# Performance work log

Hardware: AMD Instinct MI355X
Metric: run time of the kernel (lower is better)

## Reference

```python
import jax, jax.numpy as jnp
import numpy as np

N_PREV = 65536
BATCH = 2048
DIM = 128


def setup_inputs() -> dict:
    key = jax.random.key(0)
    k1, k2 = jax.random.split(key)
    n = N_PREV + BATCH
    target_lib = jax.random.normal(k1, (n, DIM), dtype=jnp.float32)
    reached_lib = jax.random.normal(k2, (n, DIM), dtype=jnp.float32)
    return {
        "target_goal_embedding_library": target_lib,
        "reached_goal_embedding_library": reached_lib,
        "batch_size": BATCH,
    }


def reference(target_goal_embedding_library, reached_goal_embedding_library, batch_size):
    # slice the library: last batch_size rows are current target/reached goals
    tg = target_goal_embedding_library[-batch_size:]      # [B, D]
    rg = reached_goal_embedding_library[-batch_size:]     # [B, D]
    prev = reached_goal_embedding_library[:-batch_size]   # [N_prev, D]

    # brute-force squared euclidean distances via gram trick: [B, N_prev]
    d2 = (
        jnp.sum(tg * tg, axis=-1, keepdims=True)
        - 2.0 * tg @ prev.T
        + jnp.sum(prev * prev, axis=-1)[None, :]
    )
    idx = jnp.argmin(d2, axis=1)          # top-1 nearest neighbor ids, [B]
    closest = prev[idx]                   # [B, D] gather

    # LP(g, s, r) = ||g - s|| - ||g - r||; value and grad wrt g, vmapped over batch
    def LP(g, s, r):
        return (
            jnp.sqrt(jnp.sum(jnp.square(g - s), axis=-1))
            - jnp.sqrt(jnp.sum(jnp.square(g - r), axis=-1))
        )

    IM_vals, IM_grads = jax.vmap(jax.value_and_grad(LP, 0), in_axes=(0, 0, 0))(
        tg, closest, rg
    )
    return IM_vals, IM_grads
```

## Files before the change

kernel.cpp:

```cpp
#include <hip/hip_runtime.h>
#include <math.h>

#define DIM 128
#define BATCH 2048
#define NPREV 65536
#define NCH 64
#define NJT 16
#define DELTA 0.8f

typedef __attribute__((ext_vector_type(8))) short bf16x8;
typedef __attribute__((ext_vector_type(4))) float f32x4;
typedef unsigned short u16;

static __device__ __forceinline__ unsigned short f2bf(float f) {
    unsigned int u = __float_as_uint(f);
    u += 0x7FFF + ((u >> 16) & 1);
    return (unsigned short)(u >> 16);
}

#define GLOAD16(g, l) __builtin_amdgcn_global_load_lds( \
    (const __attribute__((address_space(1))) void*)(g), \
    (__attribute__((address_space(3))) void*)(l), 16, 0, 0)

__global__ __launch_bounds__(256) void k_convB(const float* __restrict__ src,
                                               u16* __restrict__ dst,
                                               float* __restrict__ p2part) {
    int id = blockIdx.x * 256 + threadIdx.x;
    int img = id >> 9, c = id & 511;
    int ks2 = c >> 8, rem = c & 255, col = rem >> 2, slot = rem & 3;
    int koct = slot ^ ((col >> 1) & 3);
    int srow = (img >> 1) * 64 + col;
    int scol = (img & 1) * 64 + ks2 * 32 + koct * 8;
    const float* s = src + (size_t)srow * DIM + scol;
    float4 f0 = *reinterpret_cast<const float4*>(s);
    float4 f1 = *reinterpret_cast<const float4*>(s + 4);
    float f[8] = {f0.x, f0.y, f0.z, f0.w, f1.x, f1.y, f1.z, f1.w};
    union { unsigned short us[8]; uint4 v; } o;
    float sum = 0.f;
    #pragma unroll
    for (int e = 0; e < 8; ++e) { o.us[e] = f2bf(f[e]); sum += f[e] * f[e]; }
    *reinterpret_cast<uint4*>(dst + (size_t)id * 8) = o.v;
    p2part[srow * 16 + (scol >> 3)] = sum;
}

__global__ __launch_bounds__(256) void k_prev2r(const float* __restrict__ p2part,
                                                float* __restrict__ p2h) {
    int row = blockIdx.x * 256 + threadIdx.x;
    const float4* p = reinterpret_cast<const float4*>(p2part + (size_t)row * 16);
    float4 a = p[0], b = p[1], c = p[2], d = p[3];
    float s = ((a.x + a.y) + (a.z + a.w)) + ((b.x + b.y) + (b.z + b.w))
            + ((c.x + c.y) + (c.z + c.w)) + ((d.x + d.y) + (d.z + d.w));
    p2h[row] = -0.5f * s;
}

__global__ __launch_bounds__(256) void k_convA(const float* __restrict__ src,
                                               u16* __restrict__ dst) {
    int id = blockIdx.x * 256 + threadIdx.x;
    int img = id >> 10, c = id & 1023;
    int ks2 = c >> 9, rem = c & 511, row = rem >> 2, koct = rem & 3;
    int srow = (img >> 1) * 128 + row;
    int scol = (img & 1) * 64 + ks2 * 32 + koct * 8;
    const float* s = src + (size_t)srow * DIM + scol;
    float4 f0 = *reinterpret_cast<const float4*>(s);
    float4 f1 = *reinterpret_cast<const float4*>(s + 4);
    float f[8] = {f0.x, f0.y, f0.z, f0.w, f1.x, f1.y, f1.z, f1.w};
    union { unsigned short us[8]; uint4 v; } o;
    #pragma unroll
    for (int e = 0; e < 8; ++e) o.us[e] = f2bf(f[e]);
    *reinterpret_cast<uint4*>(dst + (size_t)id * 8) = o.v;
}

__global__ __launch_bounds__(256, 3) void k_gemm_argmin(
    const u16* __restrict__ Aimg, const u16* __restrict__ Bimg,
    const float* __restrict__ p2h, float4* __restrict__ partial)
{
    __shared__ __align__(16) u16 Bt[2][8192];

    const int t = threadIdx.x;
    const int lane = t & 63;
    const int w = t >> 6;
    const int wrow = w & 1;
    const int cg = w >> 1;
    const int l15 = lane & 15;
    const int lhi = lane >> 4;

    const int bid = blockIdx.x;
    const int mtile = bid >> 6;
    const int chunk = bid & 63;

    const u16* gb0 = Bimg + (size_t)chunk * NJT * 8192;

    #pragma unroll
    for (int c = 0; c < 4; ++c)
        GLOAD16(gb0 + c * 2048 + t * 8, &Bt[0][c * 2048 + t * 8]);

    bf16x8 areg[4][4];
    {
        const u16* ab = Aimg + (size_t)mtile * 2 * 8192;
        #pragma unroll
        for (int s = 0; s < 4; ++s) {
            const int img = s >> 1, ks2 = s & 1;
            #pragma unroll
            for (int fm = 0; fm < 4; ++fm) {
                int row = wrow * 64 + fm * 16 + l15;
                areg[s][fm] = *reinterpret_cast<const bf16x8*>(
                    ab + (size_t)img * 8192 + (ks2 * 512 + row * 4 + lhi) * 8);
            }
        }
    }

    const int bbase = (cg * 32 + l15) * 64 + ((lhi ^ ((l15 >> 1) & 3)) << 4);
    const unsigned sbase = ((unsigned)cg << 8) | (unsigned)l15;
    const int phbase = chunk * 1024 + cg * 32 + l15;
    const f32x4 z4 = {0.f, 0.f, 0.f, 0.f};

    float v1[4][4], v2[4][4];
    #pragma unroll
    for (int fm = 0; fm < 4; ++fm)
        #pragma unroll
        for (int r = 0; r < 4; ++r) { v1[fm][r] = -INFINITY; v2[fm][r] = -INFINITY; }

    float phc[2];
    phc[0] = p2h[phbase]; phc[1] = p2h[phbase + 16];

    for (int jt = 0; jt < NJT; ++jt) {
        const int p = jt & 1;
        __syncthreads();
        if (jt + 1 < NJT) {
            const u16* gb = gb0 + (size_t)(jt + 1) * 8192;
            u16* lb = Bt[p ^ 1];
            #pragma unroll
            for (int c = 0; c < 4; ++c)
                GLOAD16(gb + c * 2048 + t * 8, lb + c * 2048 + t * 8);
        }
        float phn[2];
        if (jt + 1 < NJT) {
            phn[0] = p2h[phbase + (jt + 1) * 64];
            phn[1] = p2h[phbase + (jt + 1) * 64 + 16];
        }

        f32x4 acc[4][2];
        const char* Bc = (const char*)Bt[p];
        __builtin_amdgcn_s_setprio(1);
        #pragma unroll
        for (int s = 0; s < 4; ++s) {
            const int h = s >> 1, ks2 = s & 1;
            bf16x8 bf[2];
            #pragma unroll
            for (int fn = 0; fn < 2; ++fn)
                bf[fn] = *reinterpret_cast<const bf16x8*>(
                    Bc + h * 8192 + ks2 * 4096 + fn * 1024 + bbase);
            if (s == 0) {
                #pragma unroll
                for (int fm = 0; fm < 4; ++fm)
                    #pragma unroll
                    for (int fn = 0; fn < 2; ++fn)
                        acc[fm][fn] = __builtin_amdgcn_mfma_f32_16x16x32_bf16(
                            areg[0][fm], bf[fn], z4, 0, 0, 0);
            } else {
                #pragma unroll
                for (int fm = 0; fm < 4; ++fm)
                    #pragma unroll
                    for (int fn = 0; fn < 2; ++fn)
                        acc[fm][fn] = __builtin_amdgcn_mfma_f32_16x16x32_bf16(
                            areg[s][fm], bf[fn], acc[fm][fn], 0, 0, 0);
            }
        }
        __builtin_amdgcn_s_setprio(0);

        const unsigned stampv = sbase | ((unsigned)jt << 4);
        #pragma unroll
        for (int fm = 0; fm < 4; ++fm) {
            #pragma unroll
            for (int r = 0; r < 4; ++r) {
                float s0 = acc[fm][0][r] + phc[0];
                float s1 = acc[fm][1][r] + phc[1];
                float m = fmaxf(s0, s1);
                float key = __uint_as_float((__float_as_uint(m) & ~0x7FFu) | stampv);
                float tm = fminf(v1[fm][r], key);
                v1[fm][r] = fmaxf(v1[fm][r], key);
                v2[fm][r] = fmaxf(v2[fm][r], tm);
            }
        }

        if (jt + 1 < NJT) { phc[0] = phn[0]; phc[1] = phn[1]; }
    }

    float2* red = reinterpret_cast<float2*>(Bt);
    #pragma unroll
    for (int fm = 0; fm < 4; ++fm) {
        #pragma unroll
        for (int r = 0; r < 4; ++r) {
            float a1 = v1[fm][r], a2 = v2[fm][r];
            #pragma unroll
            for (int m = 1; m < 16; m <<= 1) {
                float o1 = __shfl_xor(a1, m), o2 = __shfl_xor(a2, m);
                float n2 = fmaxf(fminf(a1, o1), fmaxf(a2, o2));
                a1 = fmaxf(a1, o1); a2 = n2;
            }
            if (l15 == 0) {
                int row = wrow * 64 + fm * 16 + lhi * 4 + r;
                red[row * 2 + cg] = make_float2(a1, a2);
            }
        }
    }
    __syncthreads();
    if (t < 128) {
        float2 x = red[t * 2 + 0], y = red[t * 2 + 1];
        float u1f = fmaxf(x.x, y.x);
        float u2f = fmaxf(fminf(x.x, y.x), fmaxf(x.y, y.y));
        unsigned ua = __float_as_uint(u1f), ub = __float_as_uint(u2f);
        int ja = chunk * 1024 + (int)((ua >> 4) & 15) * 64 + (int)((ua >> 8) & 1) * 32
               + (int)(ua & 15);
        int jb = chunk * 1024 + (int)((ub >> 4) & 15) * 64 + (int)((ub >> 8) & 1) * 32
               + (int)(ub & 15);
        float d1 = -2.0f * __uint_as_float(ua & ~0x7FFu);
        float d2 = -2.0f * __uint_as_float(ub & ~0x7FFu);
        partial[(size_t)(mtile * 128 + t) * NCH + chunk] =
            make_float4(d1, __int_as_float(ja), d2, __int_as_float(jb));
    }
}

__global__ __launch_bounds__(256) void k_final2(
    const float* __restrict__ tg, const float* __restrict__ rg,
    const float* __restrict__ prev, const float4* __restrict__ partial,
    float* __restrict__ out_vals, float* __restrict__ out_grads)
{
    const int wv = threadIdx.x >> 6, lane = threadIdx.x & 63;
    const int i = blockIdx.x * 4 + wv;
    const float4 e = partial[(size_t)i * NCH + lane];

    float bv = e.x;
    #pragma unroll
    for (int m = 1; m < 64; m <<= 1) bv = fminf(bv, __shfl_xor(bv, m));

    unsigned long long m1 = __ballot(e.x <= bv + DELTA);
    unsigned long long m2 = __ballot(e.z <= bv + DELTA);
    const float2 g = *reinterpret_cast<const float2*>(tg + (size_t)i * DIM + 2 * lane);
    const int j1i = __float_as_int(e.y), j2i = __float_as_int(e.w);

    float bestd = INFINITY; int bestj = 0x7fffffff;
    while (m1 | m2) {
        int j0;
        if (m1) { int src = __ffsll(m1) - 1; m1 &= m1 - 1; j0 = __shfl(j1i, src); }
        else    { int src = __ffsll(m2) - 1; m2 &= m2 - 1; j0 = __shfl(j2i, src); }
        #pragma unroll
        for (int f = 0; f < 2; ++f) {
            int cj = j0 + f * 16;
            const float2 p = *reinterpret_cast<const float2*>(prev + (size_t)cj * DIM + 2 * lane);
            float dx = g.x - p.x, dy = g.y - p.y;
            float d = dx * dx + dy * dy;
            #pragma unroll
            for (int m = 1; m < 64; m <<= 1) d += __shfl_xor(d, m);
            if (d < bestd || (d == bestd && cj < bestj)) { bestd = d; bestj = cj; }
        }
    }

    const float2 s = *reinterpret_cast<const float2*>(prev + (size_t)bestj * DIM + 2 * lane);
    const float2 r = *reinterpret_cast<const float2*>(rg + (size_t)i * DIM + 2 * lane);
    const float dsx = g.x - s.x, dsy = g.y - s.y;
    const float drx = g.x - r.x, dry = g.y - r.y;
    float ds = dsx * dsx + dsy * dsy;
    float dr = drx * drx + dry * dry;
    #pragma unroll
    for (int m = 1; m < 64; m <<= 1) { ds += __shfl_xor(ds, m); dr += __shfl_xor(dr, m); }
    const float sds = sqrtf(ds), sdr = sqrtf(dr);
    if (lane == 0) out_vals[i] = sds - sdr;
    const float is = 1.0f / sds, ir = 1.0f / sdr;
    float2 gr;
    gr.x = dsx * is - drx * ir;
    gr.y = dsy * is - dry * ir;
    *reinterpret_cast<float2*>(out_grads + (size_t)i * DIM + 2 * lane) = gr;
}

#define TM 128
#define TN 128
#define FNCHUNK 16
#define JT_PER_CHUNK 32

__global__ __launch_bounds__(256) void k_prev2(const float* __restrict__ prev,
                                               float* __restrict__ prev2,
                                               int nprev) {
    const int wave = threadIdx.x >> 6;
    const int lane = threadIdx.x & 63;
    const int row = blockIdx.x * 4 + wave;
    if (row >= nprev) return;
    const float2 v = *reinterpret_cast<const float2*>(prev + (size_t)row * DIM + 2 * lane);
    float s = v.x * v.x + v.y * v.y;
    #pragma unroll
    for (int m = 1; m < 64; m <<= 1) s += __shfl_xor(s, m);
    if (lane == 0) prev2[row] = s;
}

__global__ __launch_bounds__(256, 1) void k_argmin_fb(
    const float* __restrict__ tg, const float* __restrict__ prev,
    const float* __restrict__ prev2, float2* __restrict__ partial)
{
    __shared__ float4 tgL[TM * 32];
    __shared__ float4 pvL[TN * 32];
    __shared__ float  p2L[TN];
    const int t = threadIdx.x;
    const int rowTile = blockIdx.x;
    const int chunk = blockIdx.y;
    const float4* tgG = reinterpret_cast<const float4*>(tg + (size_t)rowTile * TM * DIM);
    #pragma unroll
    for (int i = 0; i < 16; ++i) {
        const int idx = t + 256 * i;
        const int row = idx >> 5, kk = idx & 31;
        tgL[row * 32 + (kk ^ (row & 7))] = tgG[idx];
    }
    const int tx = t & 15, ty = t >> 4;
    const int sa = ty & 7, sb = tx & 7;
    float minval[8]; int minidx[8];
    #pragma unroll
    for (int ri = 0; ri < 8; ++ri) { minval[ri] = INFINITY; minidx[ri] = 0x7fffffff; }
    const int jchunk0 = chunk * (JT_PER_CHUNK * TN);
    for (int jt = 0; jt < JT_PER_CHUNK; ++jt) {
        const int j0 = jchunk0 + jt * TN;
        __syncthreads();
        const float4* pvG = reinterpret_cast<const float4*>(prev + (size_t)j0 * DIM);
        #pragma unroll
        for (int i = 0; i < 16; ++i) {
            const int idx = t + 256 * i;
            const int row = idx >> 5, kk = idx & 31;
            pvL[row * 32 + (kk ^ (row & 7))] = pvG[idx];
        }
        if (t < TN) p2L[t] = prev2[j0 + t];
        __syncthreads();
        float acc[8][8];
        #pragma unroll
        for (int ri = 0; ri < 8; ++ri)
            #pragma unroll
            for (int ci = 0; ci < 8; ++ci) acc[ri][ci] = 0.f;
        #pragma unroll 2
        for (int kk = 0; kk < 32; ++kk) {
            float4 a[8], b[8];
            const int ka = kk ^ sa, kb = kk ^ sb;
            #pragma unroll
            for (int ri = 0; ri < 8; ++ri) a[ri] = tgL[(ty + 16 * ri) * 32 + ka];
            #pragma unroll
            for (int ci = 0; ci < 8; ++ci) b[ci] = pvL[(tx + 16 * ci) * 32 + kb];
            #pragma unroll
            for (int ri = 0; ri < 8; ++ri)
                #pragma unroll
                for (int ci = 0; ci < 8; ++ci) {
                    acc[ri][ci] += a[ri].x * b[ci].x;
                    acc[ri][ci] += a[ri].y * b[ci].y;
                    acc[ri][ci] += a[ri].z * b[ci].z;
                    acc[ri][ci] += a[ri].w * b[ci].w;
                }
        }
        #pragma unroll
        for (int ci = 0; ci < 8; ++ci) {
            const int jl = tx + 16 * ci;
            const int jg = j0 + jl;
            const float pj = p2L[jl];
            #pragma unroll
            for (int ri = 0; ri < 8; ++ri) {
                const float d = pj - 2.f * acc[ri][ci];
                if (d < minval[ri]) { minval[ri] = d; minidx[ri] = jg; }
            }
        }
    }
    __syncthreads();
    float2* red = reinterpret_cast<float2*>(pvL);
    #pragma unroll
    for (int ri = 0; ri < 8; ++ri) {
        const int row = ty + 16 * ri;
        red[row * 16 + tx] = make_float2(minval[ri], __int_as_float(minidx[ri]));
    }
    __syncthreads();
    if (t < TM) {
        float bv = INFINITY; int bi = 0x7fffffff;
        #pragma unroll
        for (int e = 0; e < 16; ++e) {
            const float2 p = red[t * 16 + e];
            const int pi = __float_as_int(p.y);
            if (p.x < bv || (p.x == bv && pi < bi)) { bv = p.x; bi = pi; }
        }
        partial[(size_t)(rowTile * TM + t) * FNCHUNK + chunk] =
            make_float2(bv, __int_as_float(bi));
    }
}

__global__ __launch_bounds__(256) void k_final_fb(
    const float* __restrict__ tg, const float* __restrict__ rg,
    const float* __restrict__ prev, const float2* __restrict__ partial,
    float* __restrict__ out_vals, float* __restrict__ out_grads)
{
    const int wave = threadIdx.x >> 6, lane = threadIdx.x & 63;
    const int i = blockIdx.x * 4 + wave;
    float bv = INFINITY; int bi = 0x7fffffff;
    if (lane < FNCHUNK) {
        const float2 p = partial[(size_t)i * FNCHUNK + lane];
        bv = p.x; bi = __float_as_int(p.y);
    }
    #pragma unroll
    for (int m = 1; m < 16; m <<= 1) {
        const float ov = __shfl_xor(bv, m);
        const int   oi = __shfl_xor(bi, m);
        if (ov < bv || (ov == bv && oi < bi)) { bv = ov; bi = oi; }
    }
    bi = __shfl(bi, 0);
    const float2 g = *reinterpret_cast<const float2*>(tg   + (size_t)i  * DIM + 2 * lane);
    const float2 s = *reinterpret_cast<const float2*>(prev + (size_t)bi * DIM + 2 * lane);
    const float2 r = *reinterpret_cast<const float2*>(rg   + (size_t)i  * DIM + 2 * lane);
    const float dsx = g.x - s.x, dsy = g.y - s.y;
    const float drx = g.x - r.x, dry = g.y - r.y;
    float ds = dsx * dsx + dsy * dsy;
    float dr = drx * drx + dry * dry;
    #pragma unroll
    for (int m = 1; m < 64; m <<= 1) { ds += __shfl_xor(ds, m); dr += __shfl_xor(dr, m); }
    const float sds = sqrtf(ds), sdr = sqrtf(dr);
    if (lane == 0) out_vals[i] = sds - sdr;
    const float is = 1.0f / sds, ir = 1.0f / sdr;
    float2 gr;
    gr.x = dsx * is - drx * ir;
    gr.y = dsy * is - dry * ir;
    *reinterpret_cast<float2*>(out_grads + (size_t)i * DIM + 2 * lane) = gr;
}

extern "C" void kernel_launch(void* const* d_in, const int* in_sizes, int n_in,
                              void* d_out, int out_size, void* d_ws, size_t ws_size,
                              hipStream_t stream) {
    const float* target  = (const float*)d_in[0];
    const float* reached = (const float*)d_in[1];
    const int n_total = in_sizes[0] / DIM;
    const int nprev = n_total - BATCH;

    const float* tg   = target  + (size_t)nprev * DIM;
    const float* rg   = reached + (size_t)nprev * DIM;
    const float* prev = reached;

    float* out_vals  = (float*)d_out;
    float* out_grads = out_vals + BATCH;

    const size_t offB  = 0;
    const size_t offA  = (size_t)2048 * 4096 * 2;
    const size_t offP2 = offA + (size_t)32 * 8192 * 2;
    const size_t offPP = offP2 + (size_t)NPREV * 4;
    const size_t offPt = offPP + (size_t)NPREV * 16 * 4;
    const size_t need  = offPt + (size_t)BATCH * NCH * sizeof(float4);

    if (nprev == NPREV && ws_size >= need) {
        u16*    Bb      = (u16*)((char*)d_ws + offB);
        u16*    Ab      = (u16*)((char*)d_ws + offA);
        float*  p2h     = (float*)((char*)d_ws + offP2);
        float*  p2part  = (float*)((char*)d_ws + offPP);
        float4* partial = (float4*)((char*)d_ws + offPt);

        k_convB<<<(2048 * 512) / 256, 256, 0, stream>>>(prev, Bb, p2part);
        k_convA<<<(32 * 1024) / 256, 256, 0, stream>>>(tg, Ab);
        k_prev2r<<<NPREV / 256, 256, 0, stream>>>(p2part, p2h);
        k_gemm_argmin<<<1024, 256, 0, stream>>>(Ab, Bb, p2h, partial);
        k_final2<<<BATCH / 4, 256, 0, stream>>>(tg, rg, prev, partial,
                                                out_vals, out_grads);
    } else {
        float*  prev2   = (float*)d_ws;
        float2* partial = (float2*)((char*)d_ws + (size_t)nprev * sizeof(float));
        k_prev2<<<nprev / 4, 256, 0, stream>>>(prev, prev2, nprev);
        dim3 grid(BATCH / TM, FNCHUNK);
        k_argmin_fb<<<grid, 256, 0, stream>>>(tg, prev, prev2, partial);
        k_final_fb<<<BATCH / 4, 256, 0, stream>>>(tg, rg, prev, partial, out_vals, out_grads);
    }
}
```

Measured before the change: 70.12 us.

## Load B fragments directly from global into registers, drop LDS staging

Rewrites the GEMM-argmin kernel so each wave owns a 64-row strip and streams pre-swizzled B fragments straight from global memory into registers with double-buffered banks, removing LDS, syncthreads and the cross-wave reduction. The B and A conversion kernels now emit data in exact MFMA fragment order. Each wave now covers 64 columns per tile (4 fn) and the argmin key tracks 16-column groups, so the final refinement checks 4 candidates per stamp instead of 2. Grid halves to 512 blocks with occupancy 2. This trades LDS sharing for more global/L2 traffic per wave and a costlier refinement.

```diff
diff --git a/kernel.cpp b/kernel.cpp
--- a/kernel.cpp
+++ b/kernel.cpp
@@ -5,7 +5,6 @@
 #define BATCH 2048
 #define NPREV 65536
 #define NCH 64
-#define NJT 16
 #define DELTA 0.8f
 
 typedef __attribute__((ext_vector_type(8))) short bf16x8;
@@ -18,22 +17,17 @@
     return (unsigned short)(u >> 16);
 }
 
-#define GLOAD16(g, l) __builtin_amdgcn_global_load_lds( \
-    (const __attribute__((address_space(1))) void*)(g), \
-    (__attribute__((address_space(3))) void*)(l), 16, 0, 0)
-
 __global__ __launch_bounds__(256) void k_convB(const float* __restrict__ src,
                                                u16* __restrict__ dst,
                                                float* __restrict__ p2part) {
     int id = blockIdx.x * 256 + threadIdx.x;
-    int img = id >> 9, c = id & 511;
-    int ks2 = c >> 8, rem = c & 255, col = rem >> 2, slot = rem & 3;
-    int koct = slot ^ ((col >> 1) & 3);
-    int srow = (img >> 1) * 64 + col;
-    int scol = (img & 1) * 64 + ks2 * 32 + koct * 8;
-    const float* s = src + (size_t)srow * DIM + scol;
-    float4 f0 = *reinterpret_cast<const float4*>(s);
-    float4 f1 = *reinterpret_cast<const float4*>(s + 4);
+    int lane = id & 63, frag = id >> 6;
+    int fn = frag & 3, s = (frag >> 2) & 3, jt = (frag >> 4) & 15, chunk = frag >> 8;
+    int srow = chunk * 1024 + jt * 64 + fn * 16 + (lane & 15);
+    int scol = (s >> 1) * 64 + (s & 1) * 32 + (lane >> 4) * 8;
+    const float* sp = src + (size_t)srow * DIM + scol;
+    float4 f0 = *reinterpret_cast<const float4*>(sp);
+    float4 f1 = *reinterpret_cast<const float4*>(sp + 4);
     float f[8] = {f0.x, f0.y, f0.z, f0.w, f1.x, f1.y, f1.z, f1.w};
     union { unsigned short us[8]; uint4 v; } o;
     float sum = 0.f;
@@ -56,13 +50,13 @@
 __global__ __launch_bounds__(256) void k_convA(const float* __restrict__ src,
                                                u16* __restrict__ dst) {
     int id = blockIdx.x * 256 + threadIdx.x;
-    int img = id >> 10, c = id & 1023;
-    int ks2 = c >> 9, rem = c & 511, row = rem >> 2, koct = rem & 3;
-    int srow = (img >> 1) * 128 + row;
-    int scol = (img & 1) * 64 + ks2 * 32 + koct * 8;
-    const float* s = src + (size_t)srow * DIM + scol;
-    float4 f0 = *reinterpret_cast<const float4*>(s);
-    float4 f1 = *reinterpret_cast<const float4*>(s + 4);
+    int lane = id & 63, frag = id >> 6;
+    int fm = frag & 3, s = (frag >> 2) & 3, strip = frag >> 4;
+    int srow = strip * 64 + fm * 16 + (lane & 15);
+    int scol = (s >> 1) * 64 + (s & 1) * 32 + (lane >> 4) * 8;
+    const float* sp = src + (size_t)srow * DIM + scol;
+    float4 f0 = *reinterpret_cast<const float4*>(sp);
+    float4 f1 = *reinterpret_cast<const float4*>(sp + 4);
     float f[8] = {f0.x, f0.y, f0.z, f0.w, f1.x, f1.y, f1.z, f1.w};
     union { unsigned short us[8]; uint4 v; } o;
     #pragma unroll
@@ -70,48 +64,32 @@
     *reinterpret_cast<uint4*>(dst + (size_t)id * 8) = o.v;
 }
 
-__global__ __launch_bounds__(256, 3) void k_gemm_argmin(
+__global__ __launch_bounds__(256, 2) void k_gemm_argmin(
     const u16* __restrict__ Aimg, const u16* __restrict__ Bimg,
     const float* __restrict__ p2h, float4* __restrict__ partial)
 {
-    __shared__ __align__(16) u16 Bt[2][8192];
-
     const int t = threadIdx.x;
     const int lane = t & 63;
     const int w = t >> 6;
-    const int wrow = w & 1;
-    const int cg = w >> 1;
     const int l15 = lane & 15;
     const int lhi = lane >> 4;
 
     const int bid = blockIdx.x;
-    const int mtile = bid >> 6;
     const int chunk = bid & 63;
-
-    const u16* gb0 = Bimg + (size_t)chunk * NJT * 8192;
-
-    #pragma unroll
-    for (int c = 0; c < 4; ++c)
-        GLOAD16(gb0 + c * 2048 + t * 8, &Bt[0][c * 2048 + t * 8]);
+    const int strip = (bid >> 6) * 4 + w;
 
     bf16x8 areg[4][4];
     {
-        const u16* ab = Aimg + (size_t)mtile * 2 * 8192;
-        #pragma unroll
-        for (int s = 0; s < 4; ++s) {
-            const int img = s >> 1, ks2 = s & 1;
-            #pragma unroll
-            for (int fm = 0; fm < 4; ++fm) {
-                int row = wrow * 64 + fm * 16 + l15;
-                areg[s][fm] = *reinterpret_cast<const bf16x8*>(
-                    ab + (size_t)img * 8192 + (ks2 * 512 + row * 4 + lhi) * 8);
-            }
-        }
-    }
-
-    const int bbase = (cg * 32 + l15) * 64 + ((lhi ^ ((l15 >> 1) & 3)) << 4);
-    const unsigned sbase = ((unsigned)cg << 8) | (unsigned)l15;
-    const int phbase = chunk * 1024 + cg * 32 + l15;
+        const u16* ab = Aimg + ((size_t)strip * 16) * 512 + (size_t)lane * 8;
+        #pragma unroll
+        for (int s = 0; s < 4; ++s)
+            #pragma unroll
+            for (int fm = 0; fm < 4; ++fm)
+                areg[s][fm] = *reinterpret_cast<const bf16x8*>(ab + (s * 4 + fm) * 512);
+    }
+
+    const u16* gb = Bimg + ((size_t)chunk * 256) * 512 + (size_t)lane * 8;
+    const int phbase = chunk * 1024 + l15;
     const f32x4 z4 = {0.f, 0.f, 0.f, 0.f};
 
     float v1[4][4], v2[4][4];
@@ -120,73 +98,78 @@
         #pragma unroll
         for (int r = 0; r < 4; ++r) { v1[fm][r] = -INFINITY; v2[fm][r] = -INFINITY; }
 
-    float phc[2];
-    phc[0] = p2h[phbase]; phc[1] = p2h[phbase + 16];
-
-    for (int jt = 0; jt < NJT; ++jt) {
-        const int p = jt & 1;
-        __syncthreads();
-        if (jt + 1 < NJT) {
-            const u16* gb = gb0 + (size_t)(jt + 1) * 8192;
-            u16* lb = Bt[p ^ 1];
-            #pragma unroll
-            for (int c = 0; c < 4; ++c)
-                GLOAD16(gb + c * 2048 + t * 8, lb + c * 2048 + t * 8);
-        }
-        float phn[2];
-        if (jt + 1 < NJT) {
-            phn[0] = p2h[phbase + (jt + 1) * 64];
-            phn[1] = p2h[phbase + (jt + 1) * 64 + 16];
-        }
-
-        f32x4 acc[4][2];
-        const char* Bc = (const char*)Bt[p];
+    f32x4 acc[4][4];
+    bf16x8 bk0[4], bk1[4];
+
+    #pragma unroll
+    for (int fn = 0; fn < 4; ++fn)
+        bk0[fn] = *reinterpret_cast<const bf16x8*>(gb + fn * 512);
+
+#define LOADBANK(BK, G) { \
+        const u16* gp_ = gb + (size_t)(G) * 2048; \
+        BK[0] = *reinterpret_cast<const bf16x8*>(gp_); \
+        BK[1] = *reinterpret_cast<const bf16x8*>(gp_ + 512); \
+        BK[2] = *reinterpret_cast<const bf16x8*>(gp_ + 1024); \
+        BK[3] = *reinterpret_cast<const bf16x8*>(gp_ + 1536); }
+
+#define MFMA_STAGE_INIT(BK, S) \
+        _Pragma("unroll") \
+        for (int fm = 0; fm < 4; ++fm) \
+            _Pragma("unroll") \
+            for (int fn = 0; fn < 4; ++fn) \
+                acc[fm][fn] = __builtin_amdgcn_mfma_f32_16x16x32_bf16(areg[S][fm], BK[fn], z4, 0, 0, 0);
+
+#define MFMA_STAGE_ACC(BK, S) \
+        _Pragma("unroll") \
+        for (int fm = 0; fm < 4; ++fm) \
+            _Pragma("unroll") \
+            for (int fn = 0; fn < 4; ++fn) \
+                acc[fm][fn] = __builtin_amdgcn_mfma_f32_16x16x32_bf16(areg[S][fm], BK[fn], acc[fm][fn], 0, 0, 0);
+
+    for (int jt = 0; jt < 16; ++jt) {
+        const int g0 = jt * 4;
+        float ph[4];
+        #pragma unroll
+        for (int fn = 0; fn < 4; ++fn) ph[fn] = p2h[phbase + jt * 64 + fn * 16];
+
+        LOADBANK(bk1, g0 + 1);
         __builtin_amdgcn_s_setprio(1);
-        #pragma unroll
-        for (int s = 0; s < 4; ++s) {
-            const int h = s >> 1, ks2 = s & 1;
-            bf16x8 bf[2];
-            #pragma unroll
-            for (int fn = 0; fn < 2; ++fn)
-                bf[fn] = *reinterpret_cast<const bf16x8*>(
-                    Bc + h * 8192 + ks2 * 4096 + fn * 1024 + bbase);
-            if (s == 0) {
-                #pragma unroll
-                for (int fm = 0; fm < 4; ++fm)
-                    #pragma unroll
-                    for (int fn = 0; fn < 2; ++fn)
-                        acc[fm][fn] = __builtin_amdgcn_mfma_f32_16x16x32_bf16(
-                            areg[0][fm], bf[fn], z4, 0, 0, 0);
-            } else {
-                #pragma unroll
-                for (int fm = 0; fm < 4; ++fm)
-                    #pragma unroll
-                    for (int fn = 0; fn < 2; ++fn)
-                        acc[fm][fn] = __builtin_amdgcn_mfma_f32_16x16x32_bf16(
-                            areg[s][fm], bf[fn], acc[fm][fn], 0, 0, 0);
-            }
-        }
+        MFMA_STAGE_INIT(bk0, 0);
         __builtin_amdgcn_s_setprio(0);
-
-        const unsigned stampv = sbase | ((unsigned)jt << 4);
+        LOADBANK(bk0, g0 + 2);
+        __builtin_amdgcn_s_setprio(1);
+        MFMA_STAGE_ACC(bk1, 1);
+        __builtin_amdgcn_s_setprio(0);
+        LOADBANK(bk1, g0 + 3);
+        __builtin_amdgcn_s_setprio(1);
+        MFMA_STAGE_ACC(bk0, 2);
+        __builtin_amdgcn_s_setprio(0);
+        if (jt + 1 < 16) LOADBANK(bk0, g0 + 4);
+        __builtin_amdgcn_s_setprio(1);
+        MFMA_STAGE_ACC(bk1, 3);
+        __builtin_amdgcn_s_setprio(0);
+
+        const unsigned stamp = (unsigned)l15 | ((unsigned)jt << 4);
         #pragma unroll
         for (int fm = 0; fm < 4; ++fm) {
             #pragma unroll
             for (int r = 0; r < 4; ++r) {
-                float s0 = acc[fm][0][r] + phc[0];
-                float s1 = acc[fm][1][r] + phc[1];
-                float m = fmaxf(s0, s1);
-                float key = __uint_as_float((__float_as_uint(m) & ~0x7FFu) | stampv);
+                float s0 = acc[fm][0][r] + ph[0];
+                float s1 = acc[fm][1][r] + ph[1];
+                float s2 = acc[fm][2][r] + ph[2];
+                float s3 = acc[fm][3][r] + ph[3];
+                float m = fmaxf(fmaxf(s0, s1), fmaxf(s2, s3));
+                float key = __uint_as_float((__float_as_uint(m) & ~0x7FFu) | stamp);
                 float tm = fminf(v1[fm][r], key);
                 v1[fm][r] = fmaxf(v1[fm][r], key);
                 v2[fm][r] = fmaxf(v2[fm][r], tm);
             }
         }
-
-        if (jt + 1 < NJT) { phc[0] = phn[0]; phc[1] = phn[1]; }
-    }
-
-    float2* red = reinterpret_cast<float2*>(Bt);
+    }
+#undef LOADBANK
+#undef MFMA_STAGE_INIT
+#undef MFMA_STAGE_ACC
+
     #pragma unroll
     for (int fm = 0; fm < 4; ++fm) {
         #pragma unroll
@@ -199,25 +182,15 @@
                 a1 = fmaxf(a1, o1); a2 = n2;
             }
             if (l15 == 0) {
-                int row = wrow * 64 + fm * 16 + lhi * 4 + r;
-                red[row * 2 + cg] = make_float2(a1, a2);
+                unsigned ua = __float_as_uint(a1), ub = __float_as_uint(a2);
+                int row = strip * 64 + fm * 16 + lhi * 4 + r;
+                int ja = chunk * 1024 + (int)((ua >> 4) & 15) * 64 + (int)(ua & 15);
+                int jb = chunk * 1024 + (int)((ub >> 4) & 15) * 64 + (int)(ub & 15);
+                partial[(size_t)row * NCH + chunk] = make_float4(
+                    -2.0f * __uint_as_float(ua & ~0x7FFu), __int_as_float(ja),
+                    -2.0f * __uint_as_float(ub & ~0x7FFu), __int_as_float(jb));
             }
         }
-    }
-    __syncthreads();
-    if (t < 128) {
-        float2 x = red[t * 2 + 0], y = red[t * 2 + 1];
-        float u1f = fmaxf(x.x, y.x);
-        float u2f = fmaxf(fminf(x.x, y.x), fmaxf(x.y, y.y));
-        unsigned ua = __float_as_uint(u1f), ub = __float_as_uint(u2f);
-        int ja = chunk * 1024 + (int)((ua >> 4) & 15) * 64 + (int)((ua >> 8) & 1) * 32
-               + (int)(ua & 15);
-        int jb = chunk * 1024 + (int)((ub >> 4) & 15) * 64 + (int)((ub >> 8) & 1) * 32
-               + (int)(ub & 15);
-        float d1 = -2.0f * __uint_as_float(ua & ~0x7FFu);
-        float d2 = -2.0f * __uint_as_float(ub & ~0x7FFu);
-        partial[(size_t)(mtile * 128 + t) * NCH + chunk] =
-            make_float4(d1, __int_as_float(ja), d2, __int_as_float(jb));
     }
 }
 
@@ -245,7 +218,7 @@
         if (m1) { int src = __ffsll(m1) - 1; m1 &= m1 - 1; j0 = __shfl(j1i, src); }
         else    { int src = __ffsll(m2) - 1; m2 &= m2 - 1; j0 = __shfl(j2i, src); }
         #pragma unroll
-        for (int f = 0; f < 2; ++f) {
+        for (int f = 0; f < 4; ++f) {
             int cj = j0 + f * 16;
             const float2 p = *reinterpret_cast<const float2*>(prev + (size_t)cj * DIM + 2 * lane);
             float dx = g.x - p.x, dy = g.y - p.y;
@@ -436,8 +409,8 @@
     float* out_grads = out_vals + BATCH;
 
     const size_t offB  = 0;
-    const size_t offA  = (size_t)2048 * 4096 * 2;
-    const size_t offP2 = offA + (size_t)32 * 8192 * 2;
+    const size_t offA  = (size_t)16384 * 512 * 2;
+    const size_t offP2 = offA + (size_t)512 * 512 * 2;
     const size_t offPP = offP2 + (size_t)NPREV * 4;
     const size_t offPt = offPP + (size_t)NPREV * 16 * 4;
     const size_t need  = offPt + (size_t)BATCH * NCH * sizeof(float4);
@@ -449,10 +422,10 @@
         float*  p2part  = (float*)((char*)d_ws + offPP);
         float4* partial = (float4*)((char*)d_ws + offPt);
 
-        k_convB<<<(2048 * 512) / 256, 256, 0, stream>>>(prev, Bb, p2part);
-        k_convA<<<(32 * 1024) / 256, 256, 0, stream>>>(tg, Ab);
+        k_convB<<<4096, 256, 0, stream>>>(prev, Bb, p2part);
+        k_convA<<<128, 256, 0, stream>>>(tg, Ab);
         k_prev2r<<<NPREV / 256, 256, 0, stream>>>(p2part, p2h);
-        k_gemm_argmin<<<1024, 256, 0, stream>>>(Ab, Bb, p2h, partial);
+        k_gemm_argmin<<<512, 256, 0, stream>>>(Ab, Bb, p2h, partial);
         k_final2<<<BATCH / 4, 256, 0, stream>>>(tg, rg, prev, partial,
                                                 out_vals, out_grads);
     } else {
```

New measurement: 64.68 us. 7.8% less time.
